# Kernel tuning notes

Measured on AMD Instinct MI355X. Metric: run time of the kernel, lower is better.

The kernel has to match this reference:

```python
import jax, jax.numpy as jnp
import numpy as np

FS = 100.0  # sampling_rate


def _csd(x, NF):
    # CrossSpectralDensity: per-batch, all-pairs cross-correlation (torch conv1d padding='same'),
    # then rfft over time and mean over the F*F pair axis.
    B, T, F = x.shape
    left = (T - 1) // 2                      # torch 'same' padding: left=floor, right=ceil
    xpad = jnp.pad(x, ((0, 0), (left, T - 1 - left), (0, 0)))

    def per_batch(xp_b, x_b):
        # xp_b: (Tp,F) padded signals, x_b: (T,F) kernels
        lhs = xp_b.T[:, None, :]             # (F_i, 1, Tp)  signals as batch
        rhs = x_b.T[:, None, :]              # (F_j, 1, T)   kernels as out-channels
        # lax conv = cross-correlation (no flip), matching torch conv1d
        return jax.lax.conv_general_dilated(lhs, rhs, (1,), 'VALID')  # (F_i, F_j, T)

    convs = jax.vmap(per_batch)(xpad, x)                    # (B, F, F, T)
    convs = jnp.transpose(convs, (0, 3, 1, 2)).reshape(B, T, F * F)  # pair index i*F+j
    cf = jnp.fft.rfft(convs, axis=1, norm='ortho')[:, :NF, :]
    return cf.mean(axis=-1, keepdims=True)                  # (B, NF, 1)


def reference(x, W_proj, b_proj, W_gate, b_gate, mag_w, mag_b, phase_w, phase_b, ln_gamma, ln_beta):
    B, H, F = x.shape
    NF = mag_w.shape[0]                     # = H//2 + 1 (threshold = fs/2 keeps all freqs)
    hid = W_proj.shape[1]

    fft = jnp.fft.rfft(x, axis=1, norm='ortho')[:, :NF, :]  # (B, NF, F) complex
    fft = fft + _csd(x, NF)

    mag = jnp.abs(fft)
    ang = jnp.angle(fft)
    freqs = jnp.arange(NF, dtype=x.dtype) * (FS / H)        # rfftfreq(H, 1/FS)
    ff = jnp.concatenate([
        jnp.stack([mag, jnp.sin(ang), jnp.cos(ang)], axis=-1),
        jnp.broadcast_to(freqs[None, :, None, None], (B, NF, F, 1)),
    ], axis=-1)                                             # (B, NF, F, 4)

    # per-freq projection layers all share one weight (ModuleList of the same module)
    proj = jax.nn.relu(jnp.einsum('bnfk,kh->bnfh', ff, W_proj) + b_proj)  # (B, NF, F, hid)

    # cat over freq along last dim -> (B, F, NF*hid), element [.., i*hid+h] = proj[:, i, :, h]
    flat = jnp.transpose(proj, (0, 2, 1, 3)).reshape(B, F, NF * hid)
    g = flat @ W_gate + b_gate                              # (B, F, NF)
    g = g * jax.nn.sigmoid(g)                               # SimpleGate (SiLU)
    w = jnp.transpose(jax.nn.sigmoid(g), (0, 2, 1))         # (B, NF, F)

    # Complexifier per frequency (distinct weights per freq); proj is already >=0 (relu idempotent)
    m = jax.nn.relu(jnp.einsum('bnfh,nh->bnf', proj, mag_w) + mag_b[None, :, None])
    ph = 2.0 * jnp.pi * jax.nn.sigmoid(jnp.einsum('bnfh,nh->bnf', proj, phase_w) + phase_b[None, :, None])
    new_fft = m * jnp.cos(ph) + 1j * (m * jnp.sin(ph))      # (B, NF, F) complex

    wf = w * new_fft + (1.0 - w) * fft
    wf = jnp.pad(wf, ((0, 0), (0, H // 2 + 1 - NF), (0, 0)))  # no-op here (NF == H//2+1)
    recon = jnp.fft.irfft(wf, axis=1, norm='ortho')         # (B, H, F)

    # LayerNorm(input_size) over residual
    y = recon + x
    mu = y.mean(axis=-1, keepdims=True)
    var = ((y - mu) ** 2).mean(axis=-1, keepdims=True)
    return (y - mu) / jnp.sqrt(var + 1e-5) * ln_gamma + ln_beta


def setup_inputs():
    key = jax.random.key(0)
    ks = jax.random.split(key, 12)
    B, H, F, HID = 128, 512, 16, 64
    NF = H // 2 + 1  # 257
    s = 0.05
    return {
        'x': jax.random.normal(ks[0], (B, H, F), jnp.float32),
        'W_proj': jax.random.normal(ks[1], (4, HID), jnp.float32) * s,
        'b_proj': jax.random.normal(ks[2], (HID,), jnp.float32) * s,
        'W_gate': jax.random.normal(ks[3], (NF * HID, NF), jnp.float32) * 0.01,
        'b_gate': jax.random.normal(ks[4], (NF,), jnp.float32) * s,
        'mag_w': jax.random.normal(ks[5], (NF, HID), jnp.float32) * s,
        'mag_b': jax.random.normal(ks[6], (NF,), jnp.float32) * s,
        'phase_w': jax.random.normal(ks[7], (NF, HID), jnp.float32) * s,
        'phase_b': jax.random.normal(ks[8], (NF,), jnp.float32) * s,
        'ln_gamma': jnp.ones((F,), jnp.float32),
        'ln_beta': jnp.zeros((F,), jnp.float32),
    }
```

## Files before the change

kernel.cpp:

```cpp
#include <hip/hip_runtime.h>


#define NF_ 257
#define NKB 514
#define FRAGS 263168
#define SPK 16
#define SORTHO 0.04419417382f

typedef __attribute__((ext_vector_type(8))) short short8;
typedef __attribute__((ext_vector_type(4))) float floatx4;

__device__ __forceinline__ unsigned int f2bf(float x) {
  union { float f; unsigned int u; } v; v.f = x;
  return (v.u + 0x7FFFu + ((v.u >> 16) & 1u)) >> 16;
}
__device__ __forceinline__ float bf2f(unsigned int u16) {
  union { unsigned int u; float f; } v; v.u = u16 << 16;
  return v.f;
}

__global__ __launch_bounds__(256) void k_wgt(const float* __restrict__ Wg,
                                             unsigned short* __restrict__ Bf) {
  const int slot = blockIdx.x * 256 + threadIdx.x;
  const int nblk = slot / 32896;
  const int rem = slot - nblk * 32896;
  const int kb = rem >> 6, lane = rem & 63;
  const int n = nblk * 16 + (lane & 15);
  const int k0 = kb * 32 + (lane >> 4) * 8;
  unsigned int w[4];
#pragma unroll
  for (int jp = 0; jp < 4; ++jp) {
    float v0 = (n < NF_) ? Wg[(k0 + jp * 2) * NF_ + n] : 0.f;
    float v1 = (n < NF_) ? Wg[(k0 + jp * 2 + 1) * NF_ + n] : 0.f;
    w[jp] = f2bf(v0) | (f2bf(v1) << 16);
  }
  *(uint4*)(Bf + (size_t)slot * 8) = make_uint4(w[0], w[1], w[2], w[3]);
}

__global__ __launch_bounds__(256) void k_tw(unsigned short* __restrict__ TWf) {
  const int slot = blockIdx.x * 256 + threadIdx.x;
  const int tile = slot >> 10, rem = slot & 1023;
  const int ks = rem >> 6, quad = (rem >> 4) & 3, l15 = rem & 15;
  const int grow = tile * 16 + l15;
  unsigned int pk[4];
#pragma unroll
  for (int jp = 0; jp < 4; ++jp) {
    float v0 = 0.f, v1 = 0.f;
    if (grow < 514) {
      const int k = grow >> 1;
      const int t0 = ks * 32 + quad * 8 + jp * 2;
      float s0, c0, s1, c1;
      __sincosf((float)((k * t0) & 511) * 0.01227184630f, &s0, &c0);
      __sincosf((float)((k * (t0 + 1)) & 511) * 0.01227184630f, &s1, &c1);
      v0 = (grow & 1) ? -s0 * SORTHO : c0 * SORTHO;
      v1 = (grow & 1) ? -s1 * SORTHO : c1 * SORTHO;
    }
    pk[jp] = f2bf(v0) | (f2bf(v1) << 16);
  }
  *(uint4*)(TWf + slot * 8) = make_uint4(pk[0], pk[1], pk[2], pk[3]);
}

__global__ __launch_bounds__(256) void k_itw(unsigned short* __restrict__ ITWf) {
  const int slot = blockIdx.x * 256 + threadIdx.x;
  const int tile = slot / 1088, rem = slot % 1088;
  const int ks = rem >> 6, sub = rem & 63;
  const int quad = sub >> 4, l15 = sub & 15;
  const int t = tile * 16 + l15;
  unsigned int pk[4];
#pragma unroll
  for (int jp = 0; jp < 4; ++jp) {
    float v0 = 0.f, v1 = 0.f;
#pragma unroll
    for (int h = 0; h < 2; ++h) {
      const int kidx = ks * 32 + quad * 8 + jp * 2 + h;
      float v = 0.f;
      if (kidx < 514) {
        const int k = kidx >> 1;
        const float hw = (k == 0 || k == 256) ? SORTHO : 2.f * SORTHO;
        float s, c;
        __sincosf((float)((k * t) & 511) * 0.01227184630f, &s, &c);
        v = (kidx & 1) ? -s * hw : c * hw;
      }
      if (h == 0) v0 = v; else v1 = v;
    }
    pk[jp] = f2bf(v0) | (f2bf(v1) << 16);
  }
  *(uint4*)(ITWf + slot * 8) = make_uint4(pk[0], pk[1], pk[2], pk[3]);
}

__global__ __launch_bounds__(256) void k_csd(const float* __restrict__ x,
                                             float* __restrict__ csd) {
  __shared__ float sl[768];
  __shared__ float ac[257];
  __shared__ float red[4];
  const int tid = threadIdx.x, bh = blockIdx.x, bb = blockIdx.y;
  for (int t = tid; t < 768; t += 256) {
    float v = 0.f;
    if (t < 512) {
      const float4* xp = (const float4*)(x + (bb * 512 + t) * 16);
      float4 a = xp[0], b = xp[1], c = xp[2], d = xp[3];
      v = a.x + a.y + a.z + a.w + b.x + b.y + b.z + b.w +
          c.x + c.y + c.z + c.w + d.x + d.y + d.z + d.w;
    }
    sl[t] = v;
  }
  __syncthreads();
  {
    float a0 = 0.f, a1 = 0.f, a2 = 0.f, a3 = 0.f;
    for (int tau = 0; tau < 512; tau += 4) {
      float4 u = *(const float4*)&sl[tau];
      a0 = fmaf(u.x, sl[tau + tid], a0);
      a1 = fmaf(u.y, sl[tau + tid + 1], a1);
      a2 = fmaf(u.z, sl[tau + tid + 2], a2);
      a3 = fmaf(u.w, sl[tau + tid + 3], a3);
    }
    ac[tid] = (a0 + a1) + (a2 + a3);
  }
  {
    float p = sl[tid] * sl[tid + 256];
#pragma unroll
    for (int off = 32; off; off >>= 1) p += __shfl_down(p, off);
    if ((tid & 63) == 0) red[tid >> 6] = p;
  }
  __syncthreads();
  if (tid == 0) ac[256] = red[0] + red[1] + red[2] + red[3];
  __syncthreads();
  const float S1 = SORTHO / 256.f;
  const int k = bh * 129 + tid;
  const int kmax = (bh == 0) ? 129 : 128;
  if (tid < kmax) {
    float sth, cth;
    __sincosf((float)k * 0.01227184630f, &sth, &cth);
    float c = 1.f, s = 0.f, re = 0.f, im = 0.f;
    for (int t = 0; t < 512; ++t) {
      int d = t - 255;
      float ov = ac[d < 0 ? -d : d];
      re = fmaf(ov, c, re);
      im = fmaf(-ov, s, im);
      float nc = fmaf(c, cth, -s * sth);
      s = fmaf(s, cth, c * sth);
      c = nc;
    }
    *(float2*)(csd + (bb * NF_ + k) * 2) = make_float2(re * S1, im * S1);
  }
}

__global__ __launch_bounds__(512) void k_fftg(const float* __restrict__ x,
                                              const unsigned short* __restrict__ TWf,
                                              const float* __restrict__ csd,
                                              float* __restrict__ fftc) {
  __shared__ __align__(16) unsigned short Xs[16 * 512];
  const int tid = threadIdx.x, mh = blockIdx.x, bb = blockIdx.y;
#pragma unroll
  for (int it = 0; it < 16; ++it) {
    int e = it * 512 + tid;
    int f = e & 15, t = e >> 4;
    float val = x[(bb * 512 + t) * 16 + f];
    Xs[f * 512 + (((t >> 3) ^ (f & 7)) * 8) + (t & 7)] = (unsigned short)f2bf(val);
  }
  __syncthreads();
  const int lane = tid & 63, wave = tid >> 6;
  const int l15 = lane & 15, quad = lane >> 4;
  floatx4 acc0 = {0,0,0,0}, acc1 = {0,0,0,0}, acc2 = {0,0,0,0};
  const int g0 = mh * 17 + wave, g1 = g0 + 8, g2 = mh * 17 + 16;
#pragma unroll
  for (int ks = 0; ks < 16; ++ks) {
    short8 bf = *(const short8*)&Xs[l15 * 512 + (((ks * 4 + quad) ^ (l15 & 7)) * 8)];
    short8 af0 = *(const short8*)(TWf + g0 * 8192 + ks * 512 + quad * 128 + l15 * 8);
    short8 af1 = *(const short8*)(TWf + g1 * 8192 + ks * 512 + quad * 128 + l15 * 8);
    acc0 = __builtin_amdgcn_mfma_f32_16x16x32_bf16(af0, bf, acc0, 0, 0, 0);
    acc1 = __builtin_amdgcn_mfma_f32_16x16x32_bf16(af1, bf, acc1, 0, 0, 0);
    if (wave == 0) {
      short8 af2 = *(const short8*)(TWf + g2 * 8192 + ks * 512 + quad * 128 + l15 * 8);
      acc2 = __builtin_amdgcn_mfma_f32_16x16x32_bf16(af2, bf, acc2, 0, 0, 0);
    }
  }
#pragma unroll
  for (int i = 0; i < 3; ++i) {
    if (i == 2 && wave != 0) break;
    const int g = (i == 0) ? g0 : (i == 1) ? g1 : g2;
    floatx4 a = (i == 0) ? acc0 : (i == 1) ? acc1 : acc2;
#pragma unroll
    for (int r = 0; r < 4; ++r) {
      const int grow = g * 16 + quad * 4 + r;
      if (grow < 514) {
        const int k = grow >> 1, ri = grow & 1;
        fftc[((bb * NF_ + k) * 16 + l15) * 2 + ri] =
            a[r] + csd[(bb * NF_ + k) * 2 + ri];
      }
    }
  }
}

__global__ __launch_bounds__(256) void k_new(const float* __restrict__ fftc,
                                             const float* __restrict__ W_proj,
                                             const float* __restrict__ b_proj,
                                             const float* __restrict__ mag_w,
                                             const float* __restrict__ mag_b,
                                             const float* __restrict__ phase_w,
                                             const float* __restrict__ phase_b,
                                             float* __restrict__ nf,
                                             unsigned short* __restrict__ Af) {
  __shared__ float wp[256], bp[64];
  const int tid = threadIdx.x;
  wp[tid] = W_proj[tid];
  if (tid < 64) bp[tid] = b_proj[tid];
  __syncthreads();
  const int idx = blockIdx.x * 256 + tid;
  const int bn = idx >> 4, f = idx & 15;
  const int n = bn % NF_, b = bn / NF_;
  float2 z = *(const float2*)(fftc + idx * 2);
  float d = z.x * z.x + z.y * z.y;
  float ir = d > 0.f ? rsqrtf(d) : 0.f;
  float mag = d * ir;
  float sn = z.y * ir;
  float cs = d > 0.f ? z.x * ir : 1.f;
  float fr = (float)n * 0.1953125f;
  float am = 0.f, ap = 0.f;
  unsigned short* abase = Af + ((size_t)b * NKB + n * 2) * 512 + f * 8;
#pragma unroll
  for (int hg = 0; hg < 8; ++hg) {
    unsigned int w[4];
#pragma unroll
    for (int j = 0; j < 8; ++j) {
      const int h = hg * 8 + j;
      float p = fmaf(mag, wp[h], fmaf(sn, wp[64 + h], fmaf(cs, wp[128 + h],
                fmaf(fr, wp[192 + h], bp[h]))));
      p = fmaxf(p, 0.f);
      am = fmaf(p, mag_w[n * 64 + h], am);
      ap = fmaf(p, phase_w[n * 64 + h], ap);
      unsigned int pb16 = f2bf(p);
      if (j & 1) w[j >> 1] |= pb16 << 16; else w[j >> 1] = pb16;
    }
    *(uint4*)(abase + (hg >> 2) * 512 + (hg & 3) * 128) =
        make_uint4(w[0], w[1], w[2], w[3]);
  }
  float m = fmaxf(am + mag_b[n], 0.f);
  float ph = 6.28318530718f / (1.f + __expf(-(ap + phase_b[n])));
  float sp, cp;
  __sincosf(ph, &sp, &cp);
  *(float2*)(nf + idx * 2) = make_float2(m * cp, m * sp);
}

__global__ __launch_bounds__(256) void k_gemm(const unsigned short* __restrict__ Af,
                                              const unsigned short* __restrict__ Bf,
                                              unsigned short* __restrict__ gpart) {
  const int tid = threadIdx.x;
  const int sp = blockIdx.x, mg = blockIdx.y;
  const int lane = tid & 63, wn = tid >> 6;
  const int i0 = (NF_ * sp) >> 4, i1 = (NF_ * (sp + 1)) >> 4;
  const int nk = (i1 - i0) * 2;
  const unsigned short* pa = Af + (size_t)(mg * 2) * FRAGS + (size_t)(i0 * 2) * 512 + lane * 8;
  const unsigned short* pb = Bf + (size_t)(wn * 5) * FRAGS + (size_t)(i0 * 2) * 512 + lane * 8;

  floatx4 acc[2][5];
#pragma unroll
  for (int mi = 0; mi < 2; ++mi)
#pragma unroll
    for (int nn = 0; nn < 5; ++nn) acc[mi][nn] = (floatx4){0.f, 0.f, 0.f, 0.f};

  short8 aX[2], aY[2], bX[5], bY[5];
#pragma unroll
  for (int mi = 0; mi < 2; ++mi) {
    aX[mi] = *(const short8*)(pa + mi * FRAGS);
    aY[mi] = *(const short8*)(pa + mi * FRAGS + 512);
  }
#pragma unroll
  for (int nn = 0; nn < 5; ++nn) {
    bX[nn] = *(const short8*)(pb + nn * FRAGS);
    bY[nn] = *(const short8*)(pb + nn * FRAGS + 512);
  }
  const int nsteps = (nk - 2) >> 1;
  for (int s = 0; s < nsteps; ++s) {
#pragma unroll
    for (int mi = 0; mi < 2; ++mi)
#pragma unroll
      for (int nn = 0; nn < 5; ++nn)
        acc[mi][nn] = __builtin_amdgcn_mfma_f32_16x16x32_bf16(aX[mi], bX[nn],
                                                              acc[mi][nn], 0, 0, 0);
#pragma unroll
    for (int mi = 0; mi < 2; ++mi) aX[mi] = *(const short8*)(pa + mi * FRAGS + 1024);
#pragma unroll
    for (int nn = 0; nn < 5; ++nn) bX[nn] = *(const short8*)(pb + nn * FRAGS + 1024);
#pragma unroll
    for (int mi = 0; mi < 2; ++mi)
#pragma unroll
      for (int nn = 0; nn < 5; ++nn)
        acc[mi][nn] = __builtin_amdgcn_mfma_f32_16x16x32_bf16(aY[mi], bY[nn],
                                                              acc[mi][nn], 0, 0, 0);
#pragma unroll
    for (int mi = 0; mi < 2; ++mi) aY[mi] = *(const short8*)(pa + mi * FRAGS + 1536);
#pragma unroll
    for (int nn = 0; nn < 5; ++nn) bY[nn] = *(const short8*)(pb + nn * FRAGS + 1536);
    pa += 1024; pb += 1024;
  }
#pragma unroll
  for (int mi = 0; mi < 2; ++mi)
#pragma unroll
    for (int nn = 0; nn < 5; ++nn)
      acc[mi][nn] = __builtin_amdgcn_mfma_f32_16x16x32_bf16(aX[mi], bX[nn],
                                                            acc[mi][nn], 0, 0, 0);
#pragma unroll
  for (int mi = 0; mi < 2; ++mi)
#pragma unroll
    for (int nn = 0; nn < 5; ++nn)
      acc[mi][nn] = __builtin_amdgcn_mfma_f32_16x16x32_bf16(aY[mi], bY[nn],
                                                            acc[mi][nn], 0, 0, 0);

  unsigned short* gp = gpart + ((((size_t)sp * 64 + mg) * 2) * 20 + wn * 5) * 256 + lane * 4;
#pragma unroll
  for (int mi = 0; mi < 2; ++mi)
#pragma unroll
    for (int nn = 0; nn < 5; ++nn) {
      unsigned int lo = f2bf(acc[mi][nn][0]) | (f2bf(acc[mi][nn][1]) << 16);
      unsigned int hi = f2bf(acc[mi][nn][2]) | (f2bf(acc[mi][nn][3]) << 16);
      *(uint2*)(gp + (size_t)(mi * 20 + nn) * 256) = make_uint2(lo, hi);
    }
}

__global__ __launch_bounds__(256) void k_wred(const unsigned short* __restrict__ gpart,
                                              const float* __restrict__ b_gate,
                                              float* __restrict__ wbuf) {
  const int m = blockIdx.x;
  const int mg = m >> 5, mi = (m >> 4) & 1, rr = m & 15;
  const int laneb = (rr >> 2) << 4;
  const int r = rr & 3;
  for (int n = threadIdx.x; n < NF_; n += 256) {
    const int nblk = n >> 4, l15 = n & 15;
    const unsigned short* gp = gpart +
        (((size_t)mg * 2 + mi) * 20 + nblk) * 256 + (laneb + l15) * 4 + r;
    float g = b_gate[n];
#pragma unroll
    for (int s2 = 0; s2 < SPK; ++s2)
      g += bf2f((unsigned int)gp[(size_t)s2 * 655360]);
    float sg = 1.f / (1.f + __expf(-g));
    float gs = g * sg;
    wbuf[m * NF_ + n] = 1.f / (1.f + __expf(-gs));
  }
}

__global__ __launch_bounds__(512) void k_recong(const float* __restrict__ fftc,
                                                const float* __restrict__ nfb,
                                                const float* __restrict__ wbuf,
                                                const unsigned short* __restrict__ ITWf,
                                                const float* __restrict__ x,
                                                const float* __restrict__ ln_g,
                                                const float* __restrict__ ln_b,
                                                float* __restrict__ out) {
  __shared__ __align__(16) unsigned short WFs[16 * 576];
  __shared__ float wls[16 * 257];
  const int tid = threadIdx.x, th = blockIdx.x, bb = blockIdx.y;
  for (int e = tid; e < 4096; e += 512) {
    int f = e >> 8, n = e & 255;
    wls[f * 257 + n] = wbuf[(bb * 16 + f) * NF_ + n];
  }
  if (tid < 16) wls[tid * 257 + 256] = wbuf[(bb * 16 + tid) * NF_ + 256];
  __syncthreads();
#pragma unroll
  for (int it = 0; it < 17; ++it) {
    int e = it * 512 + tid;
    int f = e & 15, row = e >> 4;
    float val = 0.f;
    if (row < 514) {
      int k = row >> 1, ri = row & 1;
      int base = ((bb * NF_ + k) * 16 + f) * 2 + ri;
      float fz = fftc[base], nz = nfb[base];
      float wv = wls[f * 257 + k];
      val = fz + wv * (nz - fz);
    }
    WFs[f * 576 + (((row >> 3) ^ (f & 7)) * 8) + (row & 7)] = (unsigned short)f2bf(val);
  }
  __syncthreads();
  const int lane = tid & 63, wave = tid >> 6;
  const int l15 = lane & 15, quad = lane >> 4;
  const float gg = ln_g[l15], gb = ln_b[l15];
  floatx4 acc[2];
  acc[0] = (floatx4){0.f, 0.f, 0.f, 0.f};
  acc[1] = (floatx4){0.f, 0.f, 0.f, 0.f};
  const int tg0 = th * 16 + wave, tg1 = tg0 + 8;
#pragma unroll
  for (int ks = 0; ks < 17; ++ks) {
    short8 bf = *(const short8*)&WFs[l15 * 576 + (((ks * 4 + quad) ^ (l15 & 7)) * 8)];
    short8 af0 = *(const short8*)(ITWf + tg0 * 8704 + ks * 512 + quad * 128 + l15 * 8);
    short8 af1 = *(const short8*)(ITWf + tg1 * 8704 + ks * 512 + quad * 128 + l15 * 8);
    acc[0] = __builtin_amdgcn_mfma_f32_16x16x32_bf16(af0, bf, acc[0], 0, 0, 0);
    acc[1] = __builtin_amdgcn_mfma_f32_16x16x32_bf16(af1, bf, acc[1], 0, 0, 0);
  }
#pragma unroll
  for (int i = 0; i < 2; ++i) {
    const int tg = (i == 0) ? tg0 : tg1;
#pragma unroll
    for (int r = 0; r < 4; ++r) {
      const int t = tg * 16 + quad * 4 + r;
      float y = acc[i][r] + x[(bb * 512 + t) * 16 + l15];
      float s1 = y, s2 = y * y;
#pragma unroll
      for (int m = 1; m < 16; m <<= 1) {
        s1 += __shfl_xor(s1, m);
        s2 += __shfl_xor(s2, m);
      }
      float mu = s1 * 0.0625f;
      float var = s2 * 0.0625f - mu * mu;
      float rs = rsqrtf(var + 1e-5f);
      out[(bb * 512 + t) * 16 + l15] = (y - mu) * rs * gg + gb;
    }
  }
}

extern "C" void kernel_launch(void* const* d_in, const int* in_sizes, int n_in,
                              void* d_out, int out_size, void* d_ws, size_t ws_size,
                              hipStream_t stream) {
  const float* x = (const float*)d_in[0];
  const float* W_proj = (const float*)d_in[1];
  const float* b_proj = (const float*)d_in[2];
  const float* W_gate = (const float*)d_in[3];
  const float* b_gate = (const float*)d_in[4];
  const float* mag_w = (const float*)d_in[5];
  const float* mag_b = (const float*)d_in[6];
  const float* phase_w = (const float*)d_in[7];
  const float* phase_b = (const float*)d_in[8];
  const float* ln_g = (const float*)d_in[9];
  const float* ln_b = (const float*)d_in[10];
  float* out = (float*)d_out;
  float* ws = (float*)d_ws;

  float* fftc = ws;
  float* nfb = ws + 1052672;
  float* wbuf = ws + 2105344;
  float* csd = ws + 2631680;
  unsigned short* Afrag = (unsigned short*)(ws + 2697472);
  unsigned short* Bfrag = (unsigned short*)(ws + 19540224);
  unsigned short* gpart = (unsigned short*)(ws + 22171904);
  unsigned short* TWf = (unsigned short*)(ws + 27414784);
  unsigned short* ITWf = (unsigned short*)(ws + 27554048);

  hipLaunchKernelGGL(k_wgt, dim3(2570), dim3(256), 0, stream, W_gate, Bfrag);
  hipLaunchKernelGGL(k_tw, dim3(136), dim3(256), 0, stream, TWf);
  hipLaunchKernelGGL(k_itw, dim3(136), dim3(256), 0, stream, ITWf);
  hipLaunchKernelGGL(k_csd, dim3(2, 128), dim3(256), 0, stream, x, csd);
  hipLaunchKernelGGL(k_fftg, dim3(2, 128), dim3(512), 0, stream, x, TWf, csd, fftc);
  hipLaunchKernelGGL(k_new, dim3(2056), dim3(256), 0, stream, fftc, W_proj, b_proj,
                     mag_w, mag_b, phase_w, phase_b, nfb, Afrag);
  hipLaunchKernelGGL(k_gemm, dim3(16, 64), dim3(256), 0, stream, Afrag, Bfrag, gpart);
  hipLaunchKernelGGL(k_wred, dim3(2048), dim3(256), 0, stream, gpart, b_gate, wbuf);
  hipLaunchKernelGGL(k_recong, dim3(2, 128), dim3(512), 0, stream, fftc, nfb, wbuf,
                     ITWf, x, ln_g, ln_b, out);
}
```

Baseline: 210.5 us.

## Merge prep kernels, widen GEMM M tile, fold split-K reduction into recon

Combines the weight-packing, twiddle generation and CSD kernels into a single launch that dispatches on block index. Each GEMM block now computes four M fragments instead of two, which halves the grid and reuses each B fragment load across more MFMAs. The separate split-K reduction and gating kernel is removed: the recon kernel now sums the bf16 partials, applies the bias, silu and sigmoid, and writes the weights straight into shared memory. This drops three launches and the wbuf round trip, at the cost of higher register pressure in the GEMM and duplicated reduction work across the two recon blocks per batch.

```diff
diff --git a/kernel.cpp b/kernel.cpp
--- a/kernel.cpp
+++ b/kernel.cpp
@@ -19,129 +19,140 @@
   return v.f;
 }
 
-__global__ __launch_bounds__(256) void k_wgt(const float* __restrict__ Wg,
-                                             unsigned short* __restrict__ Bf) {
-  const int slot = blockIdx.x * 256 + threadIdx.x;
-  const int nblk = slot / 32896;
-  const int rem = slot - nblk * 32896;
-  const int kb = rem >> 6, lane = rem & 63;
-  const int n = nblk * 16 + (lane & 15);
-  const int k0 = kb * 32 + (lane >> 4) * 8;
-  unsigned int w[4];
-#pragma unroll
-  for (int jp = 0; jp < 4; ++jp) {
-    float v0 = (n < NF_) ? Wg[(k0 + jp * 2) * NF_ + n] : 0.f;
-    float v1 = (n < NF_) ? Wg[(k0 + jp * 2 + 1) * NF_ + n] : 0.f;
-    w[jp] = f2bf(v0) | (f2bf(v1) << 16);
-  }
-  *(uint4*)(Bf + (size_t)slot * 8) = make_uint4(w[0], w[1], w[2], w[3]);
-}
-
-__global__ __launch_bounds__(256) void k_tw(unsigned short* __restrict__ TWf) {
-  const int slot = blockIdx.x * 256 + threadIdx.x;
-  const int tile = slot >> 10, rem = slot & 1023;
-  const int ks = rem >> 6, quad = (rem >> 4) & 3, l15 = rem & 15;
-  const int grow = tile * 16 + l15;
-  unsigned int pk[4];
-#pragma unroll
-  for (int jp = 0; jp < 4; ++jp) {
-    float v0 = 0.f, v1 = 0.f;
-    if (grow < 514) {
-      const int k = grow >> 1;
-      const int t0 = ks * 32 + quad * 8 + jp * 2;
-      float s0, c0, s1, c1;
-      __sincosf((float)((k * t0) & 511) * 0.01227184630f, &s0, &c0);
-      __sincosf((float)((k * (t0 + 1)) & 511) * 0.01227184630f, &s1, &c1);
-      v0 = (grow & 1) ? -s0 * SORTHO : c0 * SORTHO;
-      v1 = (grow & 1) ? -s1 * SORTHO : c1 * SORTHO;
-    }
-    pk[jp] = f2bf(v0) | (f2bf(v1) << 16);
-  }
-  *(uint4*)(TWf + slot * 8) = make_uint4(pk[0], pk[1], pk[2], pk[3]);
-}
-
-__global__ __launch_bounds__(256) void k_itw(unsigned short* __restrict__ ITWf) {
-  const int slot = blockIdx.x * 256 + threadIdx.x;
-  const int tile = slot / 1088, rem = slot % 1088;
-  const int ks = rem >> 6, sub = rem & 63;
-  const int quad = sub >> 4, l15 = sub & 15;
-  const int t = tile * 16 + l15;
-  unsigned int pk[4];
-#pragma unroll
-  for (int jp = 0; jp < 4; ++jp) {
-    float v0 = 0.f, v1 = 0.f;
-#pragma unroll
-    for (int h = 0; h < 2; ++h) {
-      const int kidx = ks * 32 + quad * 8 + jp * 2 + h;
-      float v = 0.f;
-      if (kidx < 514) {
-        const int k = kidx >> 1;
-        const float hw = (k == 0 || k == 256) ? SORTHO : 2.f * SORTHO;
-        float s, c;
-        __sincosf((float)((k * t) & 511) * 0.01227184630f, &s, &c);
-        v = (kidx & 1) ? -s * hw : c * hw;
-      }
-      if (h == 0) v0 = v; else v1 = v;
-    }
-    pk[jp] = f2bf(v0) | (f2bf(v1) << 16);
-  }
-  *(uint4*)(ITWf + slot * 8) = make_uint4(pk[0], pk[1], pk[2], pk[3]);
-}
-
-__global__ __launch_bounds__(256) void k_csd(const float* __restrict__ x,
-                                             float* __restrict__ csd) {
+__global__ __launch_bounds__(256) void k_prep(const float* __restrict__ x,
+                                              const float* __restrict__ Wg,
+                                              float* __restrict__ csd,
+                                              unsigned short* __restrict__ Bf,
+                                              unsigned short* __restrict__ TWf,
+                                              unsigned short* __restrict__ ITWf) {
   __shared__ float sl[768];
   __shared__ float ac[257];
   __shared__ float red[4];
-  const int tid = threadIdx.x, bh = blockIdx.x, bb = blockIdx.y;
-  for (int t = tid; t < 768; t += 256) {
-    float v = 0.f;
-    if (t < 512) {
-      const float4* xp = (const float4*)(x + (bb * 512 + t) * 16);
-      float4 a = xp[0], b = xp[1], c = xp[2], d = xp[3];
-      v = a.x + a.y + a.z + a.w + b.x + b.y + b.z + b.w +
-          c.x + c.y + c.z + c.w + d.x + d.y + d.z + d.w;
-    }
-    sl[t] = v;
-  }
-  __syncthreads();
+  const int tid = threadIdx.x;
+  const int blk = blockIdx.x;
+
+  if (blk < 256) {
+    const int bh = blk & 1, bb = blk >> 1;
+    for (int t = tid; t < 768; t += 256) {
+      float v = 0.f;
+      if (t < 512) {
+        const float4* xp = (const float4*)(x + (bb * 512 + t) * 16);
+        float4 a = xp[0], b = xp[1], c = xp[2], d = xp[3];
+        v = a.x + a.y + a.z + a.w + b.x + b.y + b.z + b.w +
+            c.x + c.y + c.z + c.w + d.x + d.y + d.z + d.w;
+      }
+      sl[t] = v;
+    }
+    __syncthreads();
+    {
+      float a0 = 0.f, a1 = 0.f, a2 = 0.f, a3 = 0.f;
+      for (int tau = 0; tau < 512; tau += 4) {
+        float4 u = *(const float4*)&sl[tau];
+        a0 = fmaf(u.x, sl[tau + tid], a0);
+        a1 = fmaf(u.y, sl[tau + tid + 1], a1);
+        a2 = fmaf(u.z, sl[tau + tid + 2], a2);
+        a3 = fmaf(u.w, sl[tau + tid + 3], a3);
+      }
+      ac[tid] = (a0 + a1) + (a2 + a3);
+    }
+    {
+      float p = sl[tid] * sl[tid + 256];
+#pragma unroll
+      for (int off = 32; off; off >>= 1) p += __shfl_down(p, off);
+      if ((tid & 63) == 0) red[tid >> 6] = p;
+    }
+    __syncthreads();
+    if (tid == 0) ac[256] = red[0] + red[1] + red[2] + red[3];
+    __syncthreads();
+    const float S1 = SORTHO / 256.f;
+    const int k = bh * 129 + tid;
+    const int kmax = (bh == 0) ? 129 : 128;
+    if (tid < kmax) {
+      float sth, cth;
+      __sincosf((float)k * 0.01227184630f, &sth, &cth);
+      float c = 1.f, s = 0.f, re = 0.f, im = 0.f;
+      for (int t = 0; t < 512; ++t) {
+        int d = t - 255;
+        float ov = ac[d < 0 ? -d : d];
+        re = fmaf(ov, c, re);
+        im = fmaf(-ov, s, im);
+        float nc = fmaf(c, cth, -s * sth);
+        s = fmaf(s, cth, c * sth);
+        c = nc;
+      }
+      *(float2*)(csd + (bb * NF_ + k) * 2) = make_float2(re * S1, im * S1);
+    }
+    return;
+  }
+
+  if (blk < 2826) {
+    const int slot = (blk - 256) * 256 + tid;
+    const int nblk = slot / 32896;
+    const int rem = slot - nblk * 32896;
+    const int kb = rem >> 6, lane = rem & 63;
+    const int n = nblk * 16 + (lane & 15);
+    const int k0 = kb * 32 + (lane >> 4) * 8;
+    unsigned int w[4];
+#pragma unroll
+    for (int jp = 0; jp < 4; ++jp) {
+      float v0 = (n < NF_) ? Wg[(k0 + jp * 2) * NF_ + n] : 0.f;
+      float v1 = (n < NF_) ? Wg[(k0 + jp * 2 + 1) * NF_ + n] : 0.f;
+      w[jp] = f2bf(v0) | (f2bf(v1) << 16);
+    }
+    *(uint4*)(Bf + (size_t)slot * 8) = make_uint4(w[0], w[1], w[2], w[3]);
+    return;
+  }
+
+  if (blk < 2962) {
+    const int slot = (blk - 2826) * 256 + tid;
+    const int tile = slot >> 10, rem = slot & 1023;
+    const int ks = rem >> 6, quad = (rem >> 4) & 3, l15 = rem & 15;
+    const int grow = tile * 16 + l15;
+    unsigned int pk[4];
+#pragma unroll
+    for (int jp = 0; jp < 4; ++jp) {
+      float v0 = 0.f, v1 = 0.f;
+      if (grow < 514) {
+        const int k = grow >> 1;
+        const int t0 = ks * 32 + quad * 8 + jp * 2;
+        float s0, c0, s1, c1;
+        __sincosf((float)((k * t0) & 511) * 0.01227184630f, &s0, &c0);
+        __sincosf((float)((k * (t0 + 1)) & 511) * 0.01227184630f, &s1, &c1);
+        v0 = (grow & 1) ? -s0 * SORTHO : c0 * SORTHO;
+        v1 = (grow & 1) ? -s1 * SORTHO : c1 * SORTHO;
+      }
+      pk[jp] = f2bf(v0) | (f2bf(v1) << 16);
+    }
+    *(uint4*)(TWf + slot * 8) = make_uint4(pk[0], pk[1], pk[2], pk[3]);
+    return;
+  }
+
   {
-    float a0 = 0.f, a1 = 0.f, a2 = 0.f, a3 = 0.f;
-    for (int tau = 0; tau < 512; tau += 4) {
-      float4 u = *(const float4*)&sl[tau];
-      a0 = fmaf(u.x, sl[tau + tid], a0);
-      a1 = fmaf(u.y, sl[tau + tid + 1], a1);
-      a2 = fmaf(u.z, sl[tau + tid + 2], a2);
-      a3 = fmaf(u.w, sl[tau + tid + 3], a3);
-    }
-    ac[tid] = (a0 + a1) + (a2 + a3);
-  }
-  {
-    float p = sl[tid] * sl[tid + 256];
-#pragma unroll
-    for (int off = 32; off; off >>= 1) p += __shfl_down(p, off);
-    if ((tid & 63) == 0) red[tid >> 6] = p;
-  }
-  __syncthreads();
-  if (tid == 0) ac[256] = red[0] + red[1] + red[2] + red[3];
-  __syncthreads();
-  const float S1 = SORTHO / 256.f;
-  const int k = bh * 129 + tid;
-  const int kmax = (bh == 0) ? 129 : 128;
-  if (tid < kmax) {
-    float sth, cth;
-    __sincosf((float)k * 0.01227184630f, &sth, &cth);
-    float c = 1.f, s = 0.f, re = 0.f, im = 0.f;
-    for (int t = 0; t < 512; ++t) {
-      int d = t - 255;
-      float ov = ac[d < 0 ? -d : d];
-      re = fmaf(ov, c, re);
-      im = fmaf(-ov, s, im);
-      float nc = fmaf(c, cth, -s * sth);
-      s = fmaf(s, cth, c * sth);
-      c = nc;
-    }
-    *(float2*)(csd + (bb * NF_ + k) * 2) = make_float2(re * S1, im * S1);
+    const int slot = (blk - 2962) * 256 + tid;
+    const int tile = slot / 1088, rem = slot % 1088;
+    const int ks = rem >> 6, sub = rem & 63;
+    const int quad = sub >> 4, l15 = sub & 15;
+    const int t = tile * 16 + l15;
+    unsigned int pk[4];
+#pragma unroll
+    for (int jp = 0; jp < 4; ++jp) {
+      float v0 = 0.f, v1 = 0.f;
+#pragma unroll
+      for (int h = 0; h < 2; ++h) {
+        const int kidx = ks * 32 + quad * 8 + jp * 2 + h;
+        float v = 0.f;
+        if (kidx < 514) {
+          const int k = kidx >> 1;
+          const float hw = (k == 0 || k == 256) ? SORTHO : 2.f * SORTHO;
+          float s, c;
+          __sincosf((float)((k * t) & 511) * 0.01227184630f, &s, &c);
+          v = (kidx & 1) ? -s * hw : c * hw;
+        }
+        if (h == 0) v0 = v; else v1 = v;
+      }
+      pk[jp] = f2bf(v0) | (f2bf(v1) << 16);
+    }
+    *(uint4*)(ITWf + slot * 8) = make_uint4(pk[0], pk[1], pk[2], pk[3]);
   }
 }
 
@@ -246,102 +257,82 @@
                                               const unsigned short* __restrict__ Bf,
                                               unsigned short* __restrict__ gpart) {
   const int tid = threadIdx.x;
-  const int sp = blockIdx.x, mg = blockIdx.y;
+  const int sp = blockIdx.x, mgg = blockIdx.y;
   const int lane = tid & 63, wn = tid >> 6;
   const int i0 = (NF_ * sp) >> 4, i1 = (NF_ * (sp + 1)) >> 4;
   const int nk = (i1 - i0) * 2;
-  const unsigned short* pa = Af + (size_t)(mg * 2) * FRAGS + (size_t)(i0 * 2) * 512 + lane * 8;
+  const unsigned short* pa = Af + (size_t)(mgg * 4) * FRAGS + (size_t)(i0 * 2) * 512 + lane * 8;
   const unsigned short* pb = Bf + (size_t)(wn * 5) * FRAGS + (size_t)(i0 * 2) * 512 + lane * 8;
 
-  floatx4 acc[2][5];
-#pragma unroll
-  for (int mi = 0; mi < 2; ++mi)
+  floatx4 acc[4][5];
+#pragma unroll
+  for (int mi = 0; mi < 4; ++mi)
 #pragma unroll
     for (int nn = 0; nn < 5; ++nn) acc[mi][nn] = (floatx4){0.f, 0.f, 0.f, 0.f};
 
-  short8 aX[2], aY[2], bX[5], bY[5];
-#pragma unroll
-  for (int mi = 0; mi < 2; ++mi) {
-    aX[mi] = *(const short8*)(pa + mi * FRAGS);
-    aY[mi] = *(const short8*)(pa + mi * FRAGS + 512);
+  short8 aX[4], aY[4], bX[5], bY[5];
+#pragma unroll
+  for (int mi = 0; mi < 4; ++mi) {
+    aX[mi] = *(const short8*)(pa + (size_t)mi * FRAGS);
+    aY[mi] = *(const short8*)(pa + (size_t)mi * FRAGS + 512);
   }
 #pragma unroll
   for (int nn = 0; nn < 5; ++nn) {
-    bX[nn] = *(const short8*)(pb + nn * FRAGS);
-    bY[nn] = *(const short8*)(pb + nn * FRAGS + 512);
+    bX[nn] = *(const short8*)(pb + (size_t)nn * FRAGS);
+    bY[nn] = *(const short8*)(pb + (size_t)nn * FRAGS + 512);
   }
   const int nsteps = (nk - 2) >> 1;
   for (int s = 0; s < nsteps; ++s) {
 #pragma unroll
-    for (int mi = 0; mi < 2; ++mi)
+    for (int mi = 0; mi < 4; ++mi)
 #pragma unroll
       for (int nn = 0; nn < 5; ++nn)
         acc[mi][nn] = __builtin_amdgcn_mfma_f32_16x16x32_bf16(aX[mi], bX[nn],
                                                               acc[mi][nn], 0, 0, 0);
 #pragma unroll
-    for (int mi = 0; mi < 2; ++mi) aX[mi] = *(const short8*)(pa + mi * FRAGS + 1024);
-#pragma unroll
-    for (int nn = 0; nn < 5; ++nn) bX[nn] = *(const short8*)(pb + nn * FRAGS + 1024);
-#pragma unroll
-    for (int mi = 0; mi < 2; ++mi)
+    for (int mi = 0; mi < 4; ++mi) aX[mi] = *(const short8*)(pa + (size_t)mi * FRAGS + 1024);
+#pragma unroll
+    for (int nn = 0; nn < 5; ++nn) bX[nn] = *(const short8*)(pb + (size_t)nn * FRAGS + 1024);
+#pragma unroll
+    for (int mi = 0; mi < 4; ++mi)
 #pragma unroll
       for (int nn = 0; nn < 5; ++nn)
         acc[mi][nn] = __builtin_amdgcn_mfma_f32_16x16x32_bf16(aY[mi], bY[nn],
                                                               acc[mi][nn], 0, 0, 0);
 #pragma unroll
-    for (int mi = 0; mi < 2; ++mi) aY[mi] = *(const short8*)(pa + mi * FRAGS + 1536);
-#pragma unroll
-    for (int nn = 0; nn < 5; ++nn) bY[nn] = *(const short8*)(pb + nn * FRAGS + 1536);
+    for (int mi = 0; mi < 4; ++mi) aY[mi] = *(const short8*)(pa + (size_t)mi * FRAGS + 1536);
+#pragma unroll
+    for (int nn = 0; nn < 5; ++nn) bY[nn] = *(const short8*)(pb + (size_t)nn * FRAGS + 1536);
     pa += 1024; pb += 1024;
   }
 #pragma unroll
-  for (int mi = 0; mi < 2; ++mi)
+  for (int mi = 0; mi < 4; ++mi)
 #pragma unroll
     for (int nn = 0; nn < 5; ++nn)
       acc[mi][nn] = __builtin_amdgcn_mfma_f32_16x16x32_bf16(aX[mi], bX[nn],
                                                             acc[mi][nn], 0, 0, 0);
 #pragma unroll
-  for (int mi = 0; mi < 2; ++mi)
+  for (int mi = 0; mi < 4; ++mi)
 #pragma unroll
     for (int nn = 0; nn < 5; ++nn)
       acc[mi][nn] = __builtin_amdgcn_mfma_f32_16x16x32_bf16(aY[mi], bY[nn],
                                                             acc[mi][nn], 0, 0, 0);
 
-  unsigned short* gp = gpart + ((((size_t)sp * 64 + mg) * 2) * 20 + wn * 5) * 256 + lane * 4;
-#pragma unroll
-  for (int mi = 0; mi < 2; ++mi)
+#pragma unroll
+  for (int mi = 0; mi < 4; ++mi)
 #pragma unroll
     for (int nn = 0; nn < 5; ++nn) {
       unsigned int lo = f2bf(acc[mi][nn][0]) | (f2bf(acc[mi][nn][1]) << 16);
       unsigned int hi = f2bf(acc[mi][nn][2]) | (f2bf(acc[mi][nn][3]) << 16);
-      *(uint2*)(gp + (size_t)(mi * 20 + nn) * 256) = make_uint2(lo, hi);
-    }
-}
-
-__global__ __launch_bounds__(256) void k_wred(const unsigned short* __restrict__ gpart,
-                                              const float* __restrict__ b_gate,
-                                              float* __restrict__ wbuf) {
-  const int m = blockIdx.x;
-  const int mg = m >> 5, mi = (m >> 4) & 1, rr = m & 15;
-  const int laneb = (rr >> 2) << 4;
-  const int r = rr & 3;
-  for (int n = threadIdx.x; n < NF_; n += 256) {
-    const int nblk = n >> 4, l15 = n & 15;
-    const unsigned short* gp = gpart +
-        (((size_t)mg * 2 + mi) * 20 + nblk) * 256 + (laneb + l15) * 4 + r;
-    float g = b_gate[n];
-#pragma unroll
-    for (int s2 = 0; s2 < SPK; ++s2)
-      g += bf2f((unsigned int)gp[(size_t)s2 * 655360]);
-    float sg = 1.f / (1.f + __expf(-g));
-    float gs = g * sg;
-    wbuf[m * NF_ + n] = 1.f / (1.f + __expf(-gs));
-  }
+      *(uint2*)(gpart + ((((size_t)sp * 128 + mgg * 4 + mi) * 20) + wn * 5 + nn) * 256
+                + lane * 4) = make_uint2(lo, hi);
+    }
 }
 
 __global__ __launch_bounds__(512) void k_recong(const float* __restrict__ fftc,
                                                 const float* __restrict__ nfb,
-                                                const float* __restrict__ wbuf,
+                                                const unsigned short* __restrict__ gpart,
+                                                const float* __restrict__ b_gate,
                                                 const unsigned short* __restrict__ ITWf,
                                                 const float* __restrict__ x,
                                                 const float* __restrict__ ln_g,
@@ -350,11 +341,29 @@
   __shared__ __align__(16) unsigned short WFs[16 * 576];
   __shared__ float wls[16 * 257];
   const int tid = threadIdx.x, th = blockIdx.x, bb = blockIdx.y;
-  for (int e = tid; e < 4096; e += 512) {
-    int f = e >> 8, n = e & 255;
-    wls[f * 257 + n] = wbuf[(bb * 16 + f) * NF_ + n];
-  }
-  if (tid < 16) wls[tid * 257 + 256] = wbuf[(bb * 16 + tid) * NF_ + 256];
+  const unsigned short* gpb = gpart + (size_t)bb * 5120;
+  for (int t = tid; t < 1088; t += 512) {
+    const int n = ((t >> 6) << 4) + (t & 15);
+    if (n < NF_) {
+      const int quad = (t >> 4) & 3;
+      const float bg = b_gate[n];
+      float g0 = bg, g1 = bg, g2 = bg, g3 = bg;
+#pragma unroll
+      for (int s2 = 0; s2 < SPK; ++s2) {
+        uint2 v = *(const uint2*)(gpb + (size_t)s2 * 655360 + (size_t)t * 4);
+        g0 += bf2f(v.x & 0xFFFFu); g1 += bf2f(v.x >> 16);
+        g2 += bf2f(v.y & 0xFFFFu); g3 += bf2f(v.y >> 16);
+      }
+      float gv[4] = {g0, g1, g2, g3};
+#pragma unroll
+      for (int r = 0; r < 4; ++r) {
+        float g = gv[r];
+        float sg = 1.f / (1.f + __expf(-g));
+        float gs = g * sg;
+        wls[(quad * 4 + r) * 257 + n] = 1.f / (1.f + __expf(-gs));
+      }
+    }
+  }
   __syncthreads();
 #pragma unroll
   for (int it = 0; it < 17; ++it) {
@@ -426,7 +435,6 @@
 
   float* fftc = ws;
   float* nfb = ws + 1052672;
-  float* wbuf = ws + 2105344;
   float* csd = ws + 2631680;
   unsigned short* Afrag = (unsigned short*)(ws + 2697472);
   unsigned short* Bfrag = (unsigned short*)(ws + 19540224);
@@ -434,15 +442,12 @@
   unsigned short* TWf = (unsigned short*)(ws + 27414784);
   unsigned short* ITWf = (unsigned short*)(ws + 27554048);
 
-  hipLaunchKernelGGL(k_wgt, dim3(2570), dim3(256), 0, stream, W_gate, Bfrag);
-  hipLaunchKernelGGL(k_tw, dim3(136), dim3(256), 0, stream, TWf);
-  hipLaunchKernelGGL(k_itw, dim3(136), dim3(256), 0, stream, ITWf);
-  hipLaunchKernelGGL(k_csd, dim3(2, 128), dim3(256), 0, stream, x, csd);
+  hipLaunchKernelGGL(k_prep, dim3(3098), dim3(256), 0, stream,
+                     x, W_gate, csd, Bfrag, TWf, ITWf);
   hipLaunchKernelGGL(k_fftg, dim3(2, 128), dim3(512), 0, stream, x, TWf, csd, fftc);
   hipLaunchKernelGGL(k_new, dim3(2056), dim3(256), 0, stream, fftc, W_proj, b_proj,
                      mag_w, mag_b, phase_w, phase_b, nfb, Afrag);
-  hipLaunchKernelGGL(k_gemm, dim3(16, 64), dim3(256), 0, stream, Afrag, Bfrag, gpart);
-  hipLaunchKernelGGL(k_wred, dim3(2048), dim3(256), 0, stream, gpart, b_gate, wbuf);
-  hipLaunchKernelGGL(k_recong, dim3(2, 128), dim3(512), 0, stream, fftc, nfb, wbuf,
-                     ITWf, x, ln_g, ln_b, out);
-}
+  hipLaunchKernelGGL(k_gemm, dim3(16, 32), dim3(256), 0, stream, Afrag, Bfrag, gpart);
+  hipLaunchKernelGGL(k_recong, dim3(2, 128), dim3(512), 0, stream, fftc, nfb, gpart,
+                     b_gate, ITWf, x, ln_g, ln_b, out);
+}
```

Result: faster. 182.8 us (-13.2%).
